# Kernel optimization log

Measured on AMD Instinct MI355X. Metric: run time of the kernel, lower is better.

Reference implementation:

```python
import jax, jax.numpy as jnp
import numpy as np

NUM_CLASSES = 80
IGNORE = 0.5
LABEL_SMOOTH = 0.0
MAX_GT = 20
C = 5 + NUM_CLASSES
SIZES = (13, 26, 52)
BS = 64
ANCHORS = jnp.array([
    [[0.0240, 0.0313], [0.0385, 0.0721], [0.0793, 0.0553]],
    [[0.0721, 0.1466], [0.1490, 0.1082], [0.1418, 0.2861]],
    [[0.2788, 0.2163], [0.3750, 0.4760], [0.8966, 0.7837]],
], dtype=jnp.float32)
ANCH_REV = ANCHORS[::-1]  # anchors[[2,1,0]] in the torch code


def bce(p, t):
    p = jnp.clip(p, 1e-7, 1.0 - 1e-7)
    return -t * jnp.log(p) - (1.0 - t) * jnp.log(1.0 - p)


def cal_iou(b1, b2):
    tl = jnp.maximum(b1[..., 0:2] - b1[..., 2:4] / 2, b2[..., 0:2] - b2[..., 2:4] / 2)
    br = jnp.minimum(b1[..., 0:2] + b1[..., 2:4] / 2, b2[..., 0:2] + b2[..., 2:4] / 2)
    wh = jnp.maximum(br - tl, 0.0)
    inter = wh[..., 0] * wh[..., 1]
    union = b1[..., 2] * b1[..., 3] + b2[..., 2] * b2[..., 3] - inter
    return inter / jnp.clip(union, 1e-6)


def _sample_loss(preds, tflat):
    # preds: [N, C] decoded (x,y,w,h,conf,cls...); tflat: [M, C] target grid flattened
    N = preds.shape[0]
    conf_t = tflat[:, 4]
    _, idx = jax.lax.top_k(conf_t, MAX_GT)      # gather up to MAX_GT GT slots
    gts = tflat[idx]                            # [K, C]
    gmask = gts[:, 4]                           # 1.0 for real GT, 0.0 for padding
    iou = cal_iou(gts[:, None, :4], preds[None, :, :4])  # [K, N]
    best = jnp.argmax(iou, axis=-1)             # [K]
    sel = preds[best]                           # [K, C]
    reg = jnp.sum((sel[:, :4] - gts[:, :4]) ** 2, axis=-1) * (2.0 - gts[:, 2] * gts[:, 3])
    loss_reg = jnp.sum(gmask * reg)
    tar_cls = gts[:, 5:] * (1.0 - LABEL_SMOOTH) + LABEL_SMOOTH / NUM_CLASSES
    loss_cls = jnp.sum(gmask[:, None] * bce(sel[:, 5:], tar_cls))
    # noobj mask: zero at best-matched preds (valid GTs only) and at high-IoU preds
    noobj = jnp.ones(N, preds.dtype).at[best].multiply(1.0 - gmask)
    maxiou = jnp.max(iou * gmask[:, None], axis=0)  # [N]
    noobj = noobj * (maxiou < IGNORE).astype(preds.dtype)
    loss_conf = jnp.sum(gmask * bce(sel[:, 4], 1.0)) + jnp.sum(noobj * bce(preds[:, 4], 0.0))
    return loss_reg + loss_conf + loss_cls


def _scale_loss(pred, tgt, l):
    bs, lsz = pred.shape[0], pred.shape[-1]
    p = pred.reshape(bs, 3, C, lsz, lsz).transpose(0, 1, 3, 4, 2)  # [bs,3,h,w,C]
    raw_w, raw_h = p[..., 2], p[..., 3]
    s = jax.nn.sigmoid(p)
    grid = jnp.arange(lsz, dtype=p.dtype)
    x = (grid[None, None, None, :] + s[..., 0]) / lsz
    y = (grid[None, None, :, None] + s[..., 1]) / lsz
    anch = ANCH_REV[l]  # [3,2]
    w = anch[:, 0][None, :, None, None] * jnp.exp(raw_w)
    h = anch[:, 1][None, :, None, None] * jnp.exp(raw_h)
    boxes = jnp.stack([x, y, w, h], axis=-1)
    preds = jnp.concatenate([boxes, s[..., 4:5], s[..., 5:]], axis=-1).reshape(bs, -1, C)
    tflat = tgt.reshape(bs, -1, C)
    return jnp.sum(jax.vmap(_sample_loss)(preds, tflat))


def setup_inputs() -> dict:
    key = jax.random.key(0)
    ks = jax.random.split(key, 6)
    inp = {}
    for i, lsz in enumerate(SIZES):
        inp['pred%d' % i] = jax.random.normal(ks[i], (BS, 3 * C, lsz, lsz), dtype=jnp.float32)
        M = 3 * lsz * lsz
        kb, ki, kc = jax.random.split(ks[3 + i], 3)
        xywh = jax.random.uniform(kb, (BS, MAX_GT, 4), minval=0.05, maxval=0.6, dtype=jnp.float32)
        cls_idx = jax.random.randint(kc, (BS, MAX_GT), 0, NUM_CLASSES)
        entry = jnp.concatenate([xywh, jnp.ones((BS, MAX_GT, 1), jnp.float32),
                                 jax.nn.one_hot(cls_idx, NUM_CLASSES, dtype=jnp.float32)], axis=-1)
        pos = jax.random.randint(ki, (BS, MAX_GT), 0, M)
        tflat = jnp.zeros((BS, M, C), jnp.float32).at[jnp.arange(BS)[:, None], pos].set(entry)
        inp['targets%d' % i] = tflat.reshape(BS, 3, lsz, lsz, C)
    return inp


def reference(pred0, pred1, pred2, targets0, targets1, targets2):
    return (_scale_loss(pred0, targets0, 0)
            + _scale_loss(pred1, targets1, 1)
            + _scale_loss(pred2, targets2, 2))
```

## Files before the change

### kernel.cpp

```cpp
#include <hip/hip_runtime.h>

#define CC 85
#define NC 80
#define MAXGT 20
#define BSZ 64
#define IGNORE_T 0.5f
#define CHUNK 1024

#define ROWS_B  (192u*MAXGT*CC*4u)
#define KEYS_B  (192u*MAXGT*8u)
#define NOOBJ_B (192u*4u)

__constant__ float d_anch[3][3][2] = {
  {{0.2788f,0.2163f},{0.375f,0.476f},{0.8966f,0.7837f}},
  {{0.0721f,0.1466f},{0.149f,0.1082f},{0.1418f,0.2861f}},
  {{0.024f,0.0313f},{0.0385f,0.0721f},{0.0793f,0.0553f}},
};
__constant__ int d_lsz[3] = {13,26,52};

__device__ __forceinline__ float sigmoidf(float x){ return 1.0f/(1.0f+__expf(-x)); }
__device__ __forceinline__ float bcef(float p, float t){
  p = fminf(fmaxf(p, 1e-7f), 1.0f-1e-7f);
  return -t*__logf(p) - (1.0f-t)*__logf(1.0f-p);
}
__device__ __forceinline__ float iouf(float gx,float gy,float gw,float gh,
                                      float px,float py,float pw,float ph){
  float tlx = fmaxf(gx-gw*0.5f, px-pw*0.5f);
  float tly = fmaxf(gy-gh*0.5f, py-ph*0.5f);
  float brx = fminf(gx+gw*0.5f, px+pw*0.5f);
  float bry = fminf(gy+gh*0.5f, py+ph*0.5f);
  float w = fmaxf(brx-tlx, 0.0f), h = fmaxf(bry-tly, 0.0f);
  float inter = w*h;
  float uni = gw*gh + pw*ph - inter;
  return inter / fmaxf(uni, 1e-6f);
}

__global__ __launch_bounds__(1024)
void k_gather(const float* __restrict__ t0, const float* __restrict__ t1,
              const float* __restrict__ t2,
              float* __restrict__ ws_rows, unsigned long long* __restrict__ ws_keys,
              float* __restrict__ ws_noobj, int* __restrict__ ws_cnt,
              float* __restrict__ out){
  int b = blockIdx.x, s = blockIdx.y;
  int lsz = d_lsz[s], N = 3*lsz*lsz;
  const float* tgt = (s==0 ? t0 : (s==1 ? t1 : t2)) + (size_t)b*N*CC;
  int slot = s*BSZ + b;
  int tid = threadIdx.x;
  __shared__ int cnt;
  __shared__ int pos[MAXGT];
  if(tid==0) cnt = 0;
  if(slot==0 && tid==0) out[0] = 0.0f;
  if(tid<MAXGT) ws_keys[slot*MAXGT+tid] = 0ull;
  if(tid==0) ws_noobj[slot] = 0.0f;
  __syncthreads();
  for(int n=tid; n<N; n+=blockDim.x){
    float c4 = tgt[(size_t)n*CC + 4];
    if(c4 > 0.5f){ int i = atomicAdd(&cnt,1); if(i<MAXGT) pos[i]=n; }
  }
  __syncthreads();
  int G = min(cnt, MAXGT);
  if(tid==0) ws_cnt[slot] = G;
  float* rows = ws_rows + (size_t)slot*MAXGT*CC;
  for(int idx=tid; idx<MAXGT*CC; idx+=blockDim.x){
    int g = idx/CC, c = idx - g*CC;
    rows[idx] = (g<G) ? tgt[(size_t)pos[g]*CC + c] : 0.0f;
  }
}

__global__ __launch_bounds__(256, 2)
void k_main(const float* __restrict__ p0, const float* __restrict__ p1,
            const float* __restrict__ p2,
            const float* __restrict__ ws_rows,
            unsigned long long* __restrict__ ws_keys,
            float* __restrict__ ws_noobj){
  int s = blockIdx.z, b = blockIdx.y;
  int lsz = d_lsz[s], lsz2 = lsz*lsz, N = 3*lsz2;
  int n0 = blockIdx.x*CHUNK;
  if(n0 >= N) return;
  int slot = s*BSZ + b;
  const float* pred = (s==0 ? p0 : (s==1 ? p1 : p2)) + (size_t)b*3*CC*lsz2;
  int tid = threadIdx.x;
  __shared__ float gx[MAXGT], gy[MAXGT], gw[MAXGT], gh[MAXGT];
  if(tid < MAXGT){
    const float* r = ws_rows + ((size_t)slot*MAXGT + tid)*CC;
    gx[tid]=r[0]; gy[tid]=r[1]; gw[tid]=r[2]; gh[tid]=r[3];
  }
  __syncthreads();
  unsigned long long key[MAXGT];
  #pragma unroll
  for(int g=0; g<MAXGT; g++) key[g] = 0ull;
  float noobj = 0.0f;
  float inv = 1.0f/(float)lsz;
  float aw0=d_anch[s][0][0], ah0=d_anch[s][0][1];
  float aw1=d_anch[s][1][0], ah1=d_anch[s][1][1];
  float aw2=d_anch[s][2][0], ah2=d_anch[s][2][1];
  int nend = min(n0+CHUNK, N);
  for(int n=n0+tid; n<nend; n+=blockDim.x){
    int a = n/lsz2, rem = n - a*lsz2;
    int i = rem/lsz, j = rem - i*lsz;
    const float* base = pred + (size_t)a*CC*lsz2 + rem;
    float q0 = base[0];
    float q1 = base[(size_t)lsz2];
    float q2 = base[2*(size_t)lsz2];
    float q3 = base[3*(size_t)lsz2];
    float q4 = base[4*(size_t)lsz2];
    float aw = (a==0)?aw0:((a==1)?aw1:aw2);
    float ah = (a==0)?ah0:((a==1)?ah1:ah2);
    float px = ((float)j + sigmoidf(q0))*inv;
    float py = ((float)i + sigmoidf(q1))*inv;
    float pw = aw*__expf(q2);
    float ph = ah*__expf(q3);
    float maxiou = 0.0f;
    unsigned int ninv = ~(unsigned int)n;
    #pragma unroll
    for(int g=0; g<MAXGT; g++){
      float io = iouf(gx[g],gy[g],gw[g],gh[g], px,py,pw,ph);
      maxiou = fmaxf(maxiou, io);
      unsigned long long k = ((unsigned long long)__float_as_uint(io) << 32) | (unsigned long long)ninv;
      key[g] = (k > key[g]) ? k : key[g];
    }
    if(maxiou < IGNORE_T) noobj += bcef(sigmoidf(q4), 0.0f);
  }
  #pragma unroll
  for(int g=0; g<MAXGT; g++){
    unsigned long long k = key[g];
    for(int off=32; off>0; off>>=1){
      unsigned long long o = __shfl_down(k, off, 64);
      k = (o > k) ? o : k;
    }
    if((tid & 63) == 0) atomicMax(&ws_keys[slot*MAXGT+g], k);
  }
  for(int off=32; off>0; off>>=1) noobj += __shfl_down(noobj, off, 64);
  if((tid & 63) == 0) atomicAdd(&ws_noobj[slot], noobj);
}

__global__ void k_final(const float* __restrict__ p0, const float* __restrict__ p1,
                        const float* __restrict__ p2,
                        const float* __restrict__ ws_rows,
                        const unsigned long long* __restrict__ ws_keys,
                        const float* __restrict__ ws_noobj, const int* __restrict__ ws_cnt,
                        float* __restrict__ out){
  int b = blockIdx.x, s = blockIdx.y;
  int lsz = d_lsz[s], lsz2 = lsz*lsz;
  int slot = s*BSZ + b;
  const float* pred = (s==0 ? p0 : (s==1 ? p1 : p2)) + (size_t)b*3*CC*lsz2;
  const float* rows = ws_rows + (size_t)slot*MAXGT*CC;
  int tid = threadIdx.x;
  __shared__ int G_s;
  __shared__ int bn[MAXGT];
  if(tid==0) G_s = ws_cnt[slot];
  __syncthreads();
  int G = G_s;
  if(tid < G){
    unsigned long long k = ws_keys[slot*MAXGT + tid];
    bn[tid] = (int)(~(unsigned int)(k & 0xffffffffull));
  }
  __syncthreads();
  float loss = 0.0f;
  float inv = 1.0f/(float)lsz;
  if(tid < G){
    int n = bn[tid];
    int a = n/lsz2, rem = n - a*lsz2, i = rem/lsz, j = rem - i*lsz;
    const float* base = pred + (size_t)a*CC*lsz2 + rem;
    float q0 = base[0];
    float q1 = base[(size_t)lsz2];
    float q2 = base[2*(size_t)lsz2];
    float q3 = base[3*(size_t)lsz2];
    float q4 = base[4*(size_t)lsz2];
    float px = ((float)j + sigmoidf(q0))*inv;
    float py = ((float)i + sigmoidf(q1))*inv;
    float pw = d_anch[s][a][0]*__expf(q2);
    float ph = d_anch[s][a][1]*__expf(q3);
    const float* r = rows + tid*CC;
    float dx=px-r[0], dy=py-r[1], dw=pw-r[2], dh=ph-r[3];
    loss += (dx*dx + dy*dy + dw*dw + dh*dh) * (2.0f - r[2]*r[3]);
    loss += bcef(sigmoidf(q4), 1.0f);
    bool first = true;
    for(int g2=0; g2<tid; g2++) if(bn[g2]==n) first=false;
    if(first){
      float maxiou = 0.0f;
      for(int g2=0; g2<MAXGT; g2++){
        const float* r2 = rows + g2*CC;
        maxiou = fmaxf(maxiou, iouf(r2[0],r2[1],r2[2],r2[3], px,py,pw,ph));
      }
      if(maxiou < IGNORE_T) loss -= bcef(sigmoidf(q4), 0.0f);
    }
  }
  for(int idx=tid; idx<G*NC; idx+=blockDim.x){
    int g = idx/NC, c = idx - g*NC;
    int n = bn[g];
    int a = n/lsz2, rem = n - a*lsz2;
    float q = pred[(size_t)a*CC*lsz2 + (size_t)(5+c)*lsz2 + rem];
    loss += bcef(sigmoidf(q), rows[g*CC + 5 + c]);
  }
  if(tid==0) loss += ws_noobj[slot];
  __shared__ float wsum[4];
  for(int off=32; off>0; off>>=1) loss += __shfl_down(loss, off, 64);
  if((tid & 63) == 0) wsum[tid>>6] = loss;
  __syncthreads();
  if(tid==0) atomicAdd(out, wsum[0]+wsum[1]+wsum[2]+wsum[3]);
}

extern "C" void kernel_launch(void* const* d_in, const int* in_sizes, int n_in,
                              void* d_out, int out_size, void* d_ws, size_t ws_size,
                              hipStream_t stream) {
  const float* p0 = (const float*)d_in[0];
  const float* t0 = (const float*)d_in[1];
  const float* p1 = (const float*)d_in[2];
  const float* t1 = (const float*)d_in[3];
  const float* p2 = (const float*)d_in[4];
  const float* t2 = (const float*)d_in[5];
  float* out = (float*)d_out;
  char* ws = (char*)d_ws;
  float*              ws_rows  = (float*)(ws);
  unsigned long long* ws_keys  = (unsigned long long*)(ws + ROWS_B);
  float*              ws_noobj = (float*)(ws + ROWS_B + KEYS_B);
  int*                ws_cnt   = (int*)(ws + ROWS_B + KEYS_B + NOOBJ_B);

  k_gather<<<dim3(BSZ,3), 1024, 0, stream>>>(t0,t1,t2, ws_rows, ws_keys, ws_noobj, ws_cnt, out);
  k_main  <<<dim3(8,BSZ,3), 256, 0, stream>>>(p0,p1,p2, ws_rows, ws_keys, ws_noobj);
  k_final <<<dim3(BSZ,3), 256, 0, stream>>>(p0,p1,p2, ws_rows, ws_keys, ws_noobj, ws_cnt, out);
}
```

Baseline: 417.5 us.

## Replace per-sample gather kernel with grid-wide flat scan and drop row copies

The 192-block gather kernel, which scanned each sample's target grid serially with 1024 threads, is replaced by a flat scan over all target rows across many blocks. Each hit is recorded through a global atomic counter and position list. The copy of gathered GT rows into workspace is removed, and later kernels read GT boxes and class targets directly from the target tensor via the stored positions. Workspace headers and the output are now zeroed with memsets, which adds two extra launches. The order of GT slots can differ from before, but the loss sum does not depend on that order.

```diff
diff --git a/kernel.cpp b/kernel.cpp
--- a/kernel.cpp
+++ b/kernel.cpp
@@ -7,9 +7,18 @@
 #define IGNORE_T 0.5f
 #define CHUNK 1024
 
-#define ROWS_B  (192u*MAXGT*CC*4u)
+#define POS_B   (192u*MAXGT*4u)
 #define KEYS_B  (192u*MAXGT*8u)
 #define NOOBJ_B (192u*4u)
+#define HDR_B   (POS_B + KEYS_B + NOOBJ_B + 192u*4u)
+
+#define N0 507
+#define N1 2028
+#define N2 8112
+#define R0 (BSZ*N0)
+#define R1 (BSZ*N1)
+#define R2 (BSZ*N2)
+#define RTOT (R0+R1+R2)
 
 __constant__ float d_anch[3][3][2] = {
   {{0.2788f,0.2163f},{0.375f,0.476f},{0.8966f,0.7837f}},
@@ -35,42 +44,36 @@
   return inter / fmaxf(uni, 1e-6f);
 }
 
-__global__ __launch_bounds__(1024)
-void k_gather(const float* __restrict__ t0, const float* __restrict__ t1,
-              const float* __restrict__ t2,
-              float* __restrict__ ws_rows, unsigned long long* __restrict__ ws_keys,
-              float* __restrict__ ws_noobj, int* __restrict__ ws_cnt,
-              float* __restrict__ out){
-  int b = blockIdx.x, s = blockIdx.y;
-  int lsz = d_lsz[s], N = 3*lsz*lsz;
-  const float* tgt = (s==0 ? t0 : (s==1 ? t1 : t2)) + (size_t)b*N*CC;
-  int slot = s*BSZ + b;
-  int tid = threadIdx.x;
-  __shared__ int cnt;
-  __shared__ int pos[MAXGT];
-  if(tid==0) cnt = 0;
-  if(slot==0 && tid==0) out[0] = 0.0f;
-  if(tid<MAXGT) ws_keys[slot*MAXGT+tid] = 0ull;
-  if(tid==0) ws_noobj[slot] = 0.0f;
-  __syncthreads();
-  for(int n=tid; n<N; n+=blockDim.x){
-    float c4 = tgt[(size_t)n*CC + 4];
-    if(c4 > 0.5f){ int i = atomicAdd(&cnt,1); if(i<MAXGT) pos[i]=n; }
-  }
-  __syncthreads();
-  int G = min(cnt, MAXGT);
-  if(tid==0) ws_cnt[slot] = G;
-  float* rows = ws_rows + (size_t)slot*MAXGT*CC;
-  for(int idx=tid; idx<MAXGT*CC; idx+=blockDim.x){
-    int g = idx/CC, c = idx - g*CC;
-    rows[idx] = (g<G) ? tgt[(size_t)pos[g]*CC + c] : 0.0f;
-  }
+__device__ __forceinline__ void scan_hit(const float* __restrict__ t, int rl,
+                                         int Nr, int s,
+                                         int* __restrict__ ws_pos,
+                                         int* __restrict__ ws_cnt){
+  float c = t[(size_t)rl*CC + 4];
+  if(c > 0.5f){
+    int b = rl / Nr;
+    int n = rl - b*Nr;
+    int slot = s*BSZ + b;
+    int i = atomicAdd(&ws_cnt[slot], 1);
+    if(i < MAXGT) ws_pos[slot*MAXGT + i] = n;
+  }
+}
+
+__global__ __launch_bounds__(256)
+void k_scan(const float* __restrict__ t0, const float* __restrict__ t1,
+            const float* __restrict__ t2,
+            int* __restrict__ ws_pos, int* __restrict__ ws_cnt){
+  int r = blockIdx.x*256 + threadIdx.x;
+  if(r < R0)            scan_hit(t0, r,        N0, 0, ws_pos, ws_cnt);
+  else if(r < R0+R1)    scan_hit(t1, r-R0,     N1, 1, ws_pos, ws_cnt);
+  else if(r < RTOT)     scan_hit(t2, r-R0-R1,  N2, 2, ws_pos, ws_cnt);
 }
 
 __global__ __launch_bounds__(256, 2)
 void k_main(const float* __restrict__ p0, const float* __restrict__ p1,
             const float* __restrict__ p2,
-            const float* __restrict__ ws_rows,
+            const float* __restrict__ t0, const float* __restrict__ t1,
+            const float* __restrict__ t2,
+            const int* __restrict__ ws_pos, const int* __restrict__ ws_cnt,
             unsigned long long* __restrict__ ws_keys,
             float* __restrict__ ws_noobj){
   int s = blockIdx.z, b = blockIdx.y;
@@ -79,11 +82,17 @@
   if(n0 >= N) return;
   int slot = s*BSZ + b;
   const float* pred = (s==0 ? p0 : (s==1 ? p1 : p2)) + (size_t)b*3*CC*lsz2;
+  const float* tgt  = (s==0 ? t0 : (s==1 ? t1 : t2)) + (size_t)b*N*CC;
   int tid = threadIdx.x;
   __shared__ float gx[MAXGT], gy[MAXGT], gw[MAXGT], gh[MAXGT];
   if(tid < MAXGT){
-    const float* r = ws_rows + ((size_t)slot*MAXGT + tid)*CC;
-    gx[tid]=r[0]; gy[tid]=r[1]; gw[tid]=r[2]; gh[tid]=r[3];
+    int G = ws_cnt[slot];
+    float x=0.f,y=0.f,w=0.f,h=0.f;
+    if(tid < G){
+      const float* r = tgt + (size_t)ws_pos[slot*MAXGT+tid]*CC;
+      x=r[0]; y=r[1]; w=r[2]; h=r[3];
+    }
+    gx[tid]=x; gy[tid]=y; gw[tid]=w; gh[tid]=h;
   }
   __syncthreads();
   unsigned long long key[MAXGT];
@@ -95,7 +104,7 @@
   float aw1=d_anch[s][1][0], ah1=d_anch[s][1][1];
   float aw2=d_anch[s][2][0], ah2=d_anch[s][2][1];
   int nend = min(n0+CHUNK, N);
-  for(int n=n0+tid; n<nend; n+=blockDim.x){
+  for(int n=n0+tid; n<nend; n+=256){
     int a = n/lsz2, rem = n - a*lsz2;
     int i = rem/lsz, j = rem - i*lsz;
     const float* base = pred + (size_t)a*CC*lsz2 + rem;
@@ -134,26 +143,35 @@
   if((tid & 63) == 0) atomicAdd(&ws_noobj[slot], noobj);
 }
 
-__global__ void k_final(const float* __restrict__ p0, const float* __restrict__ p1,
-                        const float* __restrict__ p2,
-                        const float* __restrict__ ws_rows,
-                        const unsigned long long* __restrict__ ws_keys,
-                        const float* __restrict__ ws_noobj, const int* __restrict__ ws_cnt,
-                        float* __restrict__ out){
+__global__ __launch_bounds__(256)
+void k_final(const float* __restrict__ p0, const float* __restrict__ p1,
+             const float* __restrict__ p2,
+             const float* __restrict__ t0, const float* __restrict__ t1,
+             const float* __restrict__ t2,
+             const int* __restrict__ ws_pos, const int* __restrict__ ws_cnt,
+             const unsigned long long* __restrict__ ws_keys,
+             const float* __restrict__ ws_noobj,
+             float* __restrict__ out){
   int b = blockIdx.x, s = blockIdx.y;
-  int lsz = d_lsz[s], lsz2 = lsz*lsz;
+  int lsz = d_lsz[s], lsz2 = lsz*lsz, N = 3*lsz2;
   int slot = s*BSZ + b;
   const float* pred = (s==0 ? p0 : (s==1 ? p1 : p2)) + (size_t)b*3*CC*lsz2;
-  const float* rows = ws_rows + (size_t)slot*MAXGT*CC;
+  const float* tgt  = (s==0 ? t0 : (s==1 ? t1 : t2)) + (size_t)b*N*CC;
   int tid = threadIdx.x;
-  __shared__ int G_s;
   __shared__ int bn[MAXGT];
-  if(tid==0) G_s = ws_cnt[slot];
-  __syncthreads();
-  int G = G_s;
-  if(tid < G){
+  __shared__ int gp[MAXGT];
+  __shared__ float sx[MAXGT], sy[MAXGT], sw[MAXGT], sh[MAXGT];
+  int G = ws_cnt[slot];
+  if(tid < MAXGT){
     unsigned long long k = ws_keys[slot*MAXGT + tid];
     bn[tid] = (int)(~(unsigned int)(k & 0xffffffffull));
+    float x=0.f,y=0.f,w=0.f,h=0.f; int p=0;
+    if(tid < G){
+      p = ws_pos[slot*MAXGT + tid];
+      const float* r = tgt + (size_t)p*CC;
+      x=r[0]; y=r[1]; w=r[2]; h=r[3];
+    }
+    gp[tid]=p; sx[tid]=x; sy[tid]=y; sw[tid]=w; sh[tid]=h;
   }
   __syncthreads();
   float loss = 0.0f;
@@ -171,27 +189,25 @@
     float py = ((float)i + sigmoidf(q1))*inv;
     float pw = d_anch[s][a][0]*__expf(q2);
     float ph = d_anch[s][a][1]*__expf(q3);
-    const float* r = rows + tid*CC;
-    float dx=px-r[0], dy=py-r[1], dw=pw-r[2], dh=ph-r[3];
-    loss += (dx*dx + dy*dy + dw*dw + dh*dh) * (2.0f - r[2]*r[3]);
+    float dx=px-sx[tid], dy=py-sy[tid], dw=pw-sw[tid], dh=ph-sh[tid];
+    loss += (dx*dx + dy*dy + dw*dw + dh*dh) * (2.0f - sw[tid]*sh[tid]);
     loss += bcef(sigmoidf(q4), 1.0f);
     bool first = true;
     for(int g2=0; g2<tid; g2++) if(bn[g2]==n) first=false;
     if(first){
       float maxiou = 0.0f;
-      for(int g2=0; g2<MAXGT; g2++){
-        const float* r2 = rows + g2*CC;
-        maxiou = fmaxf(maxiou, iouf(r2[0],r2[1],r2[2],r2[3], px,py,pw,ph));
-      }
+      for(int g2=0; g2<MAXGT; g2++)
+        maxiou = fmaxf(maxiou, iouf(sx[g2],sy[g2],sw[g2],sh[g2], px,py,pw,ph));
       if(maxiou < IGNORE_T) loss -= bcef(sigmoidf(q4), 0.0f);
     }
   }
-  for(int idx=tid; idx<G*NC; idx+=blockDim.x){
+  for(int idx=tid; idx<G*NC; idx+=256){
     int g = idx/NC, c = idx - g*NC;
     int n = bn[g];
     int a = n/lsz2, rem = n - a*lsz2;
     float q = pred[(size_t)a*CC*lsz2 + (size_t)(5+c)*lsz2 + rem];
-    loss += bcef(sigmoidf(q), rows[g*CC + 5 + c]);
+    float tcls = tgt[(size_t)gp[g]*CC + 5 + c];
+    loss += bcef(sigmoidf(q), tcls);
   }
   if(tid==0) loss += ws_noobj[slot];
   __shared__ float wsum[4];
@@ -212,12 +228,17 @@
   const float* t2 = (const float*)d_in[5];
   float* out = (float*)d_out;
   char* ws = (char*)d_ws;
-  float*              ws_rows  = (float*)(ws);
-  unsigned long long* ws_keys  = (unsigned long long*)(ws + ROWS_B);
-  float*              ws_noobj = (float*)(ws + ROWS_B + KEYS_B);
-  int*                ws_cnt   = (int*)(ws + ROWS_B + KEYS_B + NOOBJ_B);
-
-  k_gather<<<dim3(BSZ,3), 1024, 0, stream>>>(t0,t1,t2, ws_rows, ws_keys, ws_noobj, ws_cnt, out);
-  k_main  <<<dim3(8,BSZ,3), 256, 0, stream>>>(p0,p1,p2, ws_rows, ws_keys, ws_noobj);
-  k_final <<<dim3(BSZ,3), 256, 0, stream>>>(p0,p1,p2, ws_rows, ws_keys, ws_noobj, ws_cnt, out);
-}
+  int*                ws_pos   = (int*)(ws);
+  unsigned long long* ws_keys  = (unsigned long long*)(ws + POS_B);
+  float*              ws_noobj = (float*)(ws + POS_B + KEYS_B);
+  int*                ws_cnt   = (int*)(ws + POS_B + KEYS_B + NOOBJ_B);
+
+  hipMemsetAsync(ws, 0, HDR_B, stream);
+  hipMemsetAsync(d_out, 0, sizeof(float), stream);
+
+  k_scan <<<(RTOT+255)/256, 256, 0, stream>>>(t0,t1,t2, ws_pos, ws_cnt);
+  k_main <<<dim3(8,BSZ,3), 256, 0, stream>>>(p0,p1,p2, t0,t1,t2,
+                                             ws_pos, ws_cnt, ws_keys, ws_noobj);
+  k_final<<<dim3(BSZ,3), 256, 0, stream>>>(p0,p1,p2, t0,t1,t2,
+                                           ws_pos, ws_cnt, ws_keys, ws_noobj, out);
+}
```

Result: no change. 417.2 us (-0.1%).
